# Optimization experiments

Measured on AMD Instinct MI355X. Metric: run time of the kernel, lower is better.

## Reference

```python
import jax, jax.numpy as jnp
import numpy as np

D, T, HID, Q = 33, 49, 64, 64


def _lin(x, w, b):
    return x @ w.T + b


def setup_inputs() -> dict:
    key = jax.random.key(0)
    ks = jax.random.split(key, 40)

    def nrm(k, shape, scale=0.1):
        return jax.random.normal(k, shape, jnp.float32) * scale

    vals = nrm(ks[0], (D, T), 1.0)
    mask = (jax.random.uniform(ks[1], (D, T)) < 0.8).astype(jnp.float32)
    delta = jax.random.uniform(ks[2], (D, T)) * 2.0
    data = jnp.stack([vals, mask, delta])  # [3, 33, 49]

    return {
        "data": data,
        "h0": nrm(ks[3], (HID,), 1.0),
        "H0": nrm(ks[4], (D, HID), 1.0),
        "gh_w": nrm(ks[5], (HID, D)), "gh_b": nrm(ks[6], (HID,)),
        "gst_w": nrm(ks[7], (HID, D)), "gst_b": nrm(ks[8], (HID,)),
        "gru_wih": nrm(ks[9], (3 * HID, D)), "gru_whh": nrm(ks[10], (3 * HID, HID)),
        "gru_bih": nrm(ks[11], (3 * HID,)), "gru_bhh": nrm(ks[12], (3 * HID,)),
        "wu0_w": nrm(ks[13], (Q, HID)), "wu0_b": nrm(ks[14], (Q,)),
        "wu1_w": nrm(ks[15], (Q, 2 * HID)), "wu1_b": nrm(ks[16], (Q,)),
        "wu_w": nrm(ks[17], (Q, 3 * HID)), "wu_b": nrm(ks[18], (Q,)),
        "wh_w": nrm(ks[19], (D, HID + Q)), "wh_b": nrm(ks[20], (D,)),
        "xst_w": nrm(ks[21], (1, HID)), "xst_b": nrm(ks[22], (1,)),
        "wrg_w": nrm(ks[23], (D, HID)),
        "wrs": nrm(ks[24], (1, HID)),
        "tWz": nrm(ks[25], (D, HID, HID)), "tUzx": nrm(ks[26], (D, HID, 1)), "tUzh": nrm(ks[27], (D, HID, HID)),
        "tWr": nrm(ks[28], (D, HID, HID)), "tUrx": nrm(ks[29], (D, HID, 1)), "tUrh": nrm(ks[30], (D, HID, HID)),
        "tWh": nrm(ks[31], (D, HID, HID)), "tUhx": nrm(ks[32], (D, HID, 1)), "tUhh": nrm(ks[33], (D, HID, HID)),
        "tbz": nrm(ks[34], (HID, 1)), "tbr": nrm(ks[35], (HID, 1)), "tbh": nrm(ks[36], (HID, 1)),
    }


def reference(data, h0, H0, gh_w, gh_b, gst_w, gst_b, gru_wih, gru_whh,
              gru_bih, gru_bhh, wu0_w, wu0_b, wu1_w, wu1_b, wu_w, wu_b,
              wh_w, wh_b, xst_w, xst_b, wrg_w, wrs, tWz, tUzx, tUzh,
              tWr, tUrx, tUrh, tWh, tUhx, tUhh, tbz, tbr, tbh):
    X, M, Dt = data[0], data[1], data[2]  # each (33, 49)
    h = h0          # (HID,) -> becomes (1, HID) after first GRUCell step
    H = H0          # (D, HID)
    outs, Hs, xps = [], [], []
    for t in range(T):
        x, m, d = X[:, t], M[:, t], Dt[:, t]
        # GRU-D style decay gate: exp(-max(0, Linear(delta)))
        gamma_h = jnp.exp(-jax.nn.relu(_lin(d, gh_w, gh_b)))
        h = gamma_h * h
        x_st = _lin(H, xst_w, xst_b).reshape(-1)       # (D,)
        x_st_c = m * x + (1 - m) * x_st                # imputed input
        # torch nn.GRUCell
        xi = x_st_c.reshape(1, D)
        hi = h.reshape(1, HID)
        gi = _lin(xi, gru_wih, gru_bih)
        gh_ = _lin(hi, gru_whh, gru_bhh)
        i_r, i_z, i_n = jnp.split(gi, 3, axis=1)
        h_r, h_z, h_n = jnp.split(gh_, 3, axis=1)
        r = jax.nn.sigmoid(i_r + h_r)
        z = jax.nn.sigmoid(i_z + h_z)
        n = jnp.tanh(i_n + r * h_n)
        h = (1 - z) * n + z * hi                       # (1, HID)
        # original detaches the history used for u_t
        outs.append(jax.lax.stop_gradient(h))
        if t == 0:
            u_t = _lin(h0.reshape(1, -1), wu0_w, wu0_b)
        elif t == 1:
            hd = jnp.concatenate([h0.reshape(1, -1), outs[0]], 0).reshape(1, -1)
            u_t = _lin(hd, wu1_w, wu1_b)
        elif t == 2:
            hd = jnp.concatenate([h0.reshape(1, -1), outs[0], outs[1]], 0).reshape(1, -1)
            u_t = _lin(hd, wu_w, wu_b)
        else:
            hd = jnp.concatenate(outs[t - 3:t], 0).reshape(1, -1)
            u_t = _lin(hd, wu_w, wu_b)
        x_gt_hat = _lin(jnp.concatenate([h, u_t], axis=1), wh_w, wh_b)  # (1, D)
        gamma_st = jnp.exp(-jax.nn.relu(_lin(d, gst_w, gst_b)))
        H = gamma_st * H
        # tMGRU cell: per-variable (D=33) batched matmuls
        Hr = H[:, :, None]              # (D, HID, 1)
        xr = x_st_c[:, None, None]      # (D, 1, 1)
        hr = h.reshape(HID, 1)          # (HID, 1)
        z_t = jax.nn.sigmoid(tWz @ Hr + tUzx @ xr + tUzh @ hr + tbz)
        r_t = jax.nn.sigmoid(tWr @ Hr + tUrx @ xr + tUrh @ hr + tbr)
        Hh = jnp.tanh(r_t * (tWh @ Hr) + tUhx @ xr + tUhh @ hr + tbh)
        H = (z_t * Hr + (1 - z_t) * Hh).reshape(D, HID)
        Hs.append(H)
        a = h @ wrg_w.T                 # (1, D)
        b = wrs @ H.T                   # (1, D)
        alpha1 = jax.nn.softmax(a / (a + b), axis=-1)
        alpha2 = jax.nn.softmax(b / (a + b), axis=-1)
        xps.append(alpha1 * x_gt_hat + alpha2 * x_st)  # (1, D)
    H_s = jnp.stack(Hs)                         # (T, D, HID)
    x_pred = jnp.concatenate(xps, axis=0).T     # (D, T)
    return H_s, x_pred
```

## Files before the change

### kernel.cpp

```cpp
#include <hip/hip_runtime.h>
#include <math.h>

#define DD 33
#define TT 49
#define HH 64
#define NB 33
#define NT 256

#define O_WIHT  0
#define O_WHHT  6336
#define O_GH    18624
#define O_GS    21760
#define O_WT0   24896
#define O_WT1   27008
#define O_WTG   31232
#define O_CU    37568
#define O_R     37700
#define O_PF    40936
#define PREP_N  37700

#define SC_AGENT __HIP_MEMORY_SCOPE_AGENT

__device__ __forceinline__ float sigm(float x) {
  return 1.f / (1.f + __expf(-x));
}
__device__ __forceinline__ float ftanh(float x) {
  x = fminf(fmaxf(x, -15.f), 15.f);
  float e = __expf(2.f * x);
  return (e - 1.f) / (e + 1.f);
}

__device__ __forceinline__ float rsum64(float v) {
#pragma unroll
  for (int o = 32; o > 0; o >>= 1) v += __shfl_xor(v, o, 64);
  return v;
}
__device__ __forceinline__ float rmax64(float v) {
#pragma unroll
  for (int o = 32; o > 0; o >>= 1) v = fmaxf(v, __shfl_xor(v, o, 64));
  return v;
}

extern "C" __global__ void gmgru_prep(
    const float* __restrict__ data, const float* __restrict__ gh_w,
    const float* __restrict__ gh_b, const float* __restrict__ gst_w,
    const float* __restrict__ gst_b, const float* __restrict__ wih,
    const float* __restrict__ whh, const float* __restrict__ wu0,
    const float* __restrict__ wu0b, const float* __restrict__ wu1,
    const float* __restrict__ wu1b, const float* __restrict__ wu,
    const float* __restrict__ wub, const float* __restrict__ wh_w,
    float* __restrict__ ws) {
  int idx = blockIdx.x * blockDim.x + threadIdx.x;
  if (idx < 6336) {
    int k = idx / 192, j = idx % 192;
    ws[O_WIHT + idx] = wih[j * DD + k];
  } else if (idx < 18624) {
    int r = idx - 6336, k = r / 192, j = r % 192;
    ws[O_WHHT + r] = whh[j * HH + k];
  } else if (idx < 21760) {
    int r = idx - 18624, t = r / 64, i = r % 64;
    float s = gh_b[i];
    for (int d2 = 0; d2 < DD; ++d2)
      s += data[2 * DD * TT + d2 * TT + t] * gh_w[i * DD + d2];
    ws[O_GH + r] = expf(-fmaxf(s, 0.f));
  } else if (idx < 24896) {
    int r = idx - 21760, t = r / 64, i = r % 64;
    float s = gst_b[i];
    for (int d2 = 0; d2 < DD; ++d2)
      s += data[2 * DD * TT + d2 * TT + t] * gst_w[i * DD + d2];
    ws[O_GS + r] = expf(-fmaxf(s, 0.f));
  } else if (idx < 27008) {
    int r = idx - 24896, dd = r / 64, k = r % 64;
    float s = 0.f;
    for (int q = 0; q < 64; ++q) s += wu0[q * 64 + k] * wh_w[dd * 128 + 64 + q];
    ws[O_WT0 + r] = s;
  } else if (idx < 31232) {
    int r = idx - 27008, dd = r / 128, k = r % 128;
    float s = 0.f;
    for (int q = 0; q < 64; ++q) s += wu1[q * 128 + k] * wh_w[dd * 128 + 64 + q];
    ws[O_WT1 + r] = s;
  } else if (idx < 37568) {
    int r = idx - 31232, dd = r / 192, k = r % 192;
    float s = 0.f;
    for (int q = 0; q < 64; ++q) s += wu[q * 192 + k] * wh_w[dd * 128 + 64 + q];
    ws[O_WTG + r] = s;
  } else if (idx < PREP_N) {
    int r = idx - 37568, dd = r / 4, v = r % 4;
    float s = 0.f;
    if (v < 3) {
      const float* bp = (v == 0) ? wu0b : (v == 1) ? wu1b : wub;
      for (int q = 0; q < 64; ++q) s += bp[q] * wh_w[dd * 128 + 64 + q];
    }
    ws[O_CU + r] = s;
  }
}

extern "C" __global__ void __launch_bounds__(NT, 1)
gmgru_main(const float* __restrict__ data, const float* __restrict__ h0,
           const float* __restrict__ H0, const float* __restrict__ bih,
           const float* __restrict__ bhh, const float* __restrict__ wh_w,
           const float* __restrict__ wh_b, const float* __restrict__ xst_w,
           const float* __restrict__ xst_b, const float* __restrict__ wrg_w,
           const float* __restrict__ wrs, const float* __restrict__ tWz,
           const float* __restrict__ tUzx, const float* __restrict__ tUzh,
           const float* __restrict__ tWr, const float* __restrict__ tUrx,
           const float* __restrict__ tUrh, const float* __restrict__ tWh,
           const float* __restrict__ tUhx, const float* __restrict__ tUhh,
           const float* __restrict__ tbz, const float* __restrict__ tbr,
           const float* __restrict__ tbh, float* __restrict__ ws,
           unsigned long long* __restrict__ pf, float* __restrict__ out) {
  __shared__ __attribute__((aligned(16))) float ubuf[3][4096];
  __shared__ float whhT_l[12288];
  __shared__ float wihT_l[6336];
  __shared__ float partW[3][4][HH], partU[3][4][HH];
  __shared__ float hpreL[HH], hnewL[HH], ghLDS[3 * HH];
  __shared__ float gpre[2][HH];
  __shared__ float xrow[TT], mrow[TT];
  __shared__ float xcddL;

  const int tid = threadIdx.x;
  const int dd = blockIdx.x;
  const int wid = tid >> 6;
  const int lane = tid & 63;

  {
    const float* usrc[3] = {tUzh, tUrh, tUhh};
#pragma unroll 1
    for (int m = 0; m < 3; ++m) {
      const float* s = usrc[m] + dd * 4096;
#pragma unroll
      for (int c = 0; c < 4; ++c) {
        int f = tid * 16 + c * 4;
        float4 v = *reinterpret_cast<const float4*>(s + f);
        int i = f >> 6, k = f & 63;
        *reinterpret_cast<float4*>(&ubuf[m][(k >> 2) * 256 + i * 4]) = v;
      }
    }
  }
  for (int i = tid; i < 12288; i += NT) whhT_l[i] = ws[O_WHHT + i];
  for (int i = tid; i < 6336; i += NT) wihT_l[i] = ws[O_WIHT + i];
  if (tid < HH) {
    gpre[0][tid] = ws[O_GH + tid];
    gpre[1][tid] = ws[O_GS + tid];
  }
  if (tid < TT) {
    xrow[tid] = data[dd * TT + tid];
    mrow[tid] = data[DD * TT + dd * TT + tid];
  }
  const float bih_r = bih[lane];
  const float bih_z = bih[64 + lane];
  const float bih_n = bih[128 + lane];
  const float bhh_r = (tid < 192) ? bhh[tid] : 0.f;
  const float ux0 = tUzx[dd * HH + lane];
  const float ux1 = tUrx[dd * HH + lane];
  const float ux2 = tUhx[dd * HH + lane];
  const float tb0 = tbz[lane];
  const float tb1 = tbr[lane];
  const float tb2 = tbh[lane];
  const float xstw_r = xst_w[lane];
  const float wrg_r = wrg_w[dd * HH + lane];
  const float wrs_r = wrs[lane];
  const float whr0_r = wh_w[dd * 128 + lane];
  const float wtg0_r = ws[O_WTG + dd * 192 + lane];
  const float wtg1_r = ws[O_WTG + dd * 192 + 64 + lane];
  const float wtg2_r = ws[O_WTG + dd * 192 + 128 + lane];
  const float wt0_r = ws[O_WT0 + dd * 64 + lane];
  const float wt1a_r = ws[O_WT1 + dd * 128 + lane];
  const float wt1b_r = ws[O_WT1 + dd * 128 + 64 + lane];
  const float cu0_r = ws[O_CU + dd * 4 + 0];
  const float cu1_r = ws[O_CU + dd * 4 + 1];
  const float cu2_r = ws[O_CU + dd * 4 + 2];
  const float whb_r = wh_b[dd];
  const float xstb_r = xst_b[0];
  const float h0s_r = h0[lane];
  float hprev = h0s_r;
  float Hrow = H0[dd * HH + lane];
  __syncthreads();

  float xst_cur = rsum64(Hrow * xstw_r) + xstb_r;
  if (wid == 0 && lane == 0) {
    float xc0 = mrow[0] * xrow[0] + (1.f - mrow[0]) * xst_cur;
    unsigned long long pk0 =
        (1ULL << 32) | (unsigned long long)__float_as_uint(xc0);
    __hip_atomic_store(&pf[dd], pk0, __ATOMIC_RELAXED, SC_AGENT);
  }
  float xg_m1 = 0.f, xg_m2 = 0.f, xs_m1 = 0.f, xs_m2 = 0.f;
  float h1 = 0.f, h2 = 0.f, h3 = 0.f;

  for (int t = 0; t < TT; ++t) {
    __syncthreads();
    float hpre_r = gpre[0][lane] * hprev;
    float Hdec_r = gpre[1][lane] * Hrow;
    if (wid == 0) hpreL[lane] = hpre_r;
    __syncthreads();

    {
      float pw0 = 0.f, pw1 = 0.f, pw2 = 0.f;
      const int base = dd * 4096 + lane * 64 + wid * 16;
#pragma unroll
      for (int g = 0; g < 4; ++g) {
        float4 a = *reinterpret_cast<const float4*>(tWz + base + g * 4);
        float4 bb = *reinterpret_cast<const float4*>(tWr + base + g * 4);
        float4 c = *reinterpret_cast<const float4*>(tWh + base + g * 4);
        float v0 = __shfl(Hdec_r, wid * 16 + g * 4 + 0, 64);
        float v1 = __shfl(Hdec_r, wid * 16 + g * 4 + 1, 64);
        float v2 = __shfl(Hdec_r, wid * 16 + g * 4 + 2, 64);
        float v3 = __shfl(Hdec_r, wid * 16 + g * 4 + 3, 64);
        pw0 += a.x * v0 + a.y * v1 + a.z * v2 + a.w * v3;
        pw1 += bb.x * v0 + bb.y * v1 + bb.z * v2 + bb.w * v3;
        pw2 += c.x * v0 + c.y * v1 + c.z * v2 + c.w * v3;
      }
      partW[0][wid][lane] = pw0;
      partW[1][wid][lane] = pw1;
      partW[2][wid][lane] = pw2;
    }
    if (tid < 3 * HH) {
      float a0 = 0.f, a1 = 0.f, a2 = 0.f, a3 = 0.f;
#pragma unroll
      for (int k = 0; k < HH; k += 4) {
        a0 += whhT_l[(k + 0) * 192 + tid] * hpreL[k + 0];
        a1 += whhT_l[(k + 1) * 192 + tid] * hpreL[k + 1];
        a2 += whhT_l[(k + 2) * 192 + tid] * hpreL[k + 2];
        a3 += whhT_l[(k + 3) * 192 + tid] * hpreL[k + 3];
      }
      ghLDS[tid] = bhh_r + ((a0 + a1) + (a2 + a3));
    }
    __syncthreads();

    float hn = 0.f;
    if (wid == 0) {
      const unsigned tagv = (unsigned)(t + 1);
      unsigned long long pk;
      for (;;) {
        pk = (lane < NB)
                 ? __hip_atomic_load(&pf[(size_t)t * NB + lane],
                                     __ATOMIC_RELAXED, SC_AGENT)
                 : (((unsigned long long)tagv) << 32);
        if (__all((int)((unsigned)(pk >> 32) == tagv))) break;
        __builtin_amdgcn_s_sleep(1);
      }
      float xcv = __uint_as_float((unsigned)(pk & 0xFFFFFFFFull));
      asm volatile("" ::: "memory");
      float gr = bih_r, gz = bih_z, gn = bih_n;
#pragma unroll
      for (int k = 0; k < DD; ++k) {
        float xk = __shfl(xcv, k, 64);
        gr += wihT_l[k * 192 + lane] * xk;
        gz += wihT_l[k * 192 + 64 + lane] * xk;
        gn += wihT_l[k * 192 + 128 + lane] * xk;
      }
      float rg = sigm(gr + ghLDS[lane]);
      float zg = sigm(gz + ghLDS[64 + lane]);
      float ng = ftanh(gn + rg * ghLDS[128 + lane]);
      hn = (1.f - zg) * ng + zg * hpre_r;
      hnewL[lane] = hn;
      float xcd = __shfl(xcv, dd, 64);
      if (lane == 0) xcddL = xcd;
    }
    __syncthreads();

    {
      float hv[16];
#pragma unroll
      for (int j = 0; j < 16; ++j) hv[j] = hnewL[wid * 16 + j];
      float pu0 = 0.f, pu1 = 0.f, pu2 = 0.f;
#pragma unroll
      for (int g = 0; g < 4; ++g) {
        const int kg = (wid * 4 + g) * 256 + lane * 4;
        float4 a = *reinterpret_cast<const float4*>(&ubuf[0][kg]);
        float4 bb = *reinterpret_cast<const float4*>(&ubuf[1][kg]);
        float4 c = *reinterpret_cast<const float4*>(&ubuf[2][kg]);
        const float v0 = hv[g * 4 + 0], v1 = hv[g * 4 + 1];
        const float v2 = hv[g * 4 + 2], v3 = hv[g * 4 + 3];
        pu0 += a.x * v0 + a.y * v1 + a.z * v2 + a.w * v3;
        pu1 += bb.x * v0 + bb.y * v1 + bb.z * v2 + bb.w * v3;
        pu2 += c.x * v0 + c.y * v1 + c.z * v2 + c.w * v3;
      }
      partU[0][wid][lane] = pu0;
      partU[1][wid][lane] = pu1;
      partU[2][wid][lane] = pu2;
    }
    __syncthreads();

    float r1v = -INFINITY, r2v = -INFINITY;
    if (wid == 1 && t >= 2 && lane < DD) {
      r1v = __hip_atomic_load(&ws[O_R + (t - 2) * 66 + lane], __ATOMIC_RELAXED,
                              SC_AGENT);
      r2v = __hip_atomic_load(&ws[O_R + (t - 2) * 66 + 33 + lane],
                              __ATOMIC_RELAXED, SC_AGENT);
    }

    float sz = partW[0][0][lane] + partW[0][1][lane] + partW[0][2][lane] +
               partW[0][3][lane] + partU[0][0][lane] + partU[0][1][lane] +
               partU[0][2][lane] + partU[0][3][lane];
    float sr = partW[1][0][lane] + partW[1][1][lane] + partW[1][2][lane] +
               partW[1][3][lane] + partU[1][0][lane] + partU[1][1][lane] +
               partU[1][2][lane] + partU[1][3][lane];
    float swh = partW[2][0][lane] + partW[2][1][lane] + partW[2][2][lane] +
                partW[2][3][lane];
    float suh = partU[2][0][lane] + partU[2][1][lane] + partU[2][2][lane] +
                partU[2][3][lane];
    float xc = xcddL;
    float z2 = sigm(sz + ux0 * xc + tb0);
    float r2g = sigm(sr + ux1 * xc + tb1);
    float hh = ftanh(r2g * swh + ux2 * xc + suh + tb2);
    float Hn = z2 * Hdec_r + (1.f - z2) * hh;
    if (wid != 0) hn = hnewL[lane];

    if (wid == 0) {
      float xsn = rsum64(xstw_r * Hn);
      if (lane == 0 && t < TT - 1) {
        float xstv = xsn + xstb_r;
        float xcn = mrow[t + 1] * xrow[t + 1] + (1.f - mrow[t + 1]) * xstv;
        unsigned long long pkn =
            (((unsigned long long)(unsigned)(t + 2)) << 32) |
            (unsigned long long)__float_as_uint(xcn);
        __hip_atomic_store(&pf[(size_t)(t + 1) * NB + dd], pkn,
                           __ATOMIC_RELAXED, SC_AGENT);
      }
    } else if (wid == 1) {
      if (t >= 2) {
        float m1 = rmax64(r1v), m2 = rmax64(r2v);
        float e1 = (lane < DD) ? __expf(r1v - m1) : 0.f;
        float e2 = (lane < DD) ? __expf(r2v - m2) : 0.f;
        float s1 = rsum64(e1), s2 = rsum64(e2);
        float r1o = __shfl(r1v, dd, 64);
        float r2o = __shfl(r2v, dd, 64);
        if (lane == 0) {
          float a1 = __expf(r1o - m1) / s1;
          float a2 = __expf(r2o - m2) / s2;
          out[TT * DD * HH + dd * TT + (t - 2)] = a1 * xg_m2 + a2 * xs_m2;
        }
      }
      float xg = whr0_r * hn;
      if (t == 0) {
        xg += wt0_r * h0s_r;
      } else if (t == 1) {
        xg += wt1a_r * h0s_r + wt1b_r * h1;
      } else if (t == 2) {
        xg += wtg0_r * h0s_r + wtg1_r * h2 + wtg2_r * h1;
      } else {
        xg += wtg0_r * h3 + wtg1_r * h2 + wtg2_r * h1;
      }
      float xgt = rsum64(xg);
      float cu = (t == 0) ? cu0_r : (t == 1) ? cu1_r : cu2_r;
      float xsn1 = rsum64(xstw_r * Hn);
      xg_m2 = xg_m1;
      xs_m2 = xs_m1;
      xg_m1 = xgt + whb_r + cu;
      xs_m1 = xst_cur;
      xst_cur = xsn1 + xstb_r;
      h3 = h2;
      h2 = h1;
      h1 = hn;
    } else if (wid == 2) {
      float av = rsum64(wrg_r * hn);
      float bvv = rsum64(wrs_r * Hn);
      if (lane == 0) {
        float s = av + bvv;
        __hip_atomic_store(&ws[O_R + t * 66 + dd], av / s, __ATOMIC_RELAXED,
                           SC_AGENT);
        __hip_atomic_store(&ws[O_R + t * 66 + 33 + dd], bvv / s,
                           __ATOMIC_RELAXED, SC_AGENT);
      }
      asm volatile("s_waitcnt vmcnt(0)" ::: "memory");
    } else {
      out[t * DD * HH + dd * HH + lane] = Hn;
      if (t + 1 < TT && lane < HH) {
        gpre[0][lane] = ws[O_GH + (t + 1) * HH + lane];
        gpre[1][lane] = ws[O_GS + (t + 1) * HH + lane];
      }
    }
    hprev = hn;
    Hrow = Hn;
  }

  __syncthreads();
  if (wid == 0 && lane == 0) {
    __hip_atomic_store(&pf[(size_t)TT * NB + dd],
                       (((unsigned long long)(unsigned)(TT + 1)) << 32),
                       __ATOMIC_RELAXED, SC_AGENT);
  }
  if (wid == 1) {
    const unsigned tagv = (unsigned)(TT + 1);
    for (;;) {
      unsigned long long pk =
          (lane < NB) ? __hip_atomic_load(&pf[(size_t)TT * NB + lane],
                                          __ATOMIC_RELAXED, SC_AGENT)
                      : (((unsigned long long)tagv) << 32);
      if (__all((int)((unsigned)(pk >> 32) == tagv))) break;
      __builtin_amdgcn_s_sleep(1);
    }
    asm volatile("" ::: "memory");
#pragma unroll 1
    for (int e = 0; e < 2; ++e) {
      const int step = TT - 2 + e;
      float r1v = -INFINITY, r2v = -INFINITY;
      if (lane < DD) {
        r1v = __hip_atomic_load(&ws[O_R + step * 66 + lane], __ATOMIC_RELAXED,
                                SC_AGENT);
        r2v = __hip_atomic_load(&ws[O_R + step * 66 + 33 + lane],
                                __ATOMIC_RELAXED, SC_AGENT);
      }
      float m1 = rmax64(r1v), m2 = rmax64(r2v);
      float e1 = (lane < DD) ? __expf(r1v - m1) : 0.f;
      float e2 = (lane < DD) ? __expf(r2v - m2) : 0.f;
      float s1 = rsum64(e1), s2 = rsum64(e2);
      float r1o = __shfl(r1v, dd, 64);
      float r2o = __shfl(r2v, dd, 64);
      if (lane == 0) {
        float a1 = __expf(r1o - m1) / s1;
        float a2 = __expf(r2o - m2) / s2;
        float xgv = (e == 0) ? xg_m2 : xg_m1;
        float xsv = (e == 0) ? xs_m2 : xs_m1;
        out[TT * DD * HH + dd * TT + step] = a1 * xgv + a2 * xsv;
      }
    }
  }
}

extern "C" void kernel_launch(void* const* d_in, const int* in_sizes, int n_in,
                              void* d_out, int out_size, void* d_ws,
                              size_t ws_size, hipStream_t stream) {
  (void)in_sizes; (void)n_in; (void)out_size; (void)ws_size;
  const float* data   = (const float*)d_in[0];
  const float* h0     = (const float*)d_in[1];
  const float* H0     = (const float*)d_in[2];
  const float* gh_w   = (const float*)d_in[3];
  const float* gh_b   = (const float*)d_in[4];
  const float* gst_w  = (const float*)d_in[5];
  const float* gst_b  = (const float*)d_in[6];
  const float* wih    = (const float*)d_in[7];
  const float* whh    = (const float*)d_in[8];
  const float* bih    = (const float*)d_in[9];
  const float* bhh    = (const float*)d_in[10];
  const float* wu0w   = (const float*)d_in[11];
  const float* wu0b   = (const float*)d_in[12];
  const float* wu1w   = (const float*)d_in[13];
  const float* wu1b   = (const float*)d_in[14];
  const float* wuw    = (const float*)d_in[15];
  const float* wub    = (const float*)d_in[16];
  const float* wh_w   = (const float*)d_in[17];
  const float* wh_b   = (const float*)d_in[18];
  const float* xst_w  = (const float*)d_in[19];
  const float* xst_b  = (const float*)d_in[20];
  const float* wrg_w  = (const float*)d_in[21];
  const float* wrs    = (const float*)d_in[22];
  const float* tWz    = (const float*)d_in[23];
  const float* tUzx   = (const float*)d_in[24];
  const float* tUzh   = (const float*)d_in[25];
  const float* tWr    = (const float*)d_in[26];
  const float* tUrx   = (const float*)d_in[27];
  const float* tUrh   = (const float*)d_in[28];
  const float* tWh    = (const float*)d_in[29];
  const float* tUhx   = (const float*)d_in[30];
  const float* tUhh   = (const float*)d_in[31];
  const float* tbz    = (const float*)d_in[32];
  const float* tbr    = (const float*)d_in[33];
  const float* tbh    = (const float*)d_in[34];

  float* ws = (float*)d_ws;
  unsigned long long* pf = (unsigned long long*)(ws + O_PF);

  hipMemsetAsync(pf, 0, (size_t)(TT + 1) * NB * 8, stream);
  gmgru_prep<<<(PREP_N + 255) / 256, 256, 0, stream>>>(
      data, gh_w, gh_b, gst_w, gst_b, wih, whh, wu0w, wu0b, wu1w, wu1b, wuw,
      wub, wh_w, ws);
  gmgru_main<<<NB, NT, 0, stream>>>(
      data, h0, H0, bih, bhh, wh_w, wh_b, xst_w, xst_b, wrg_w, wrs, tWz, tUzx,
      tUzh, tWr, tUrx, tUrh, tWh, tUhx, tUhh, tbz, tbr, tbh, ws, pf,
      (float*)d_out);
}
```

Before: 202.9 us.

## Aggregate per-step barrier through block 0 and broadcast single flag

Instead of every block polling all 33 per-block slots each step, block 0 alone gathers them with a tight spin (no sleep) and then publishes one per-step flag. The other blocks poll only that flag, then read the slots once. Slots are padded to a stride of 64 per step, and the memset now covers both the slot array and the flag array. This cuts polling traffic on contended cache lines, but adds an extra hop of latency on the serial per-step critical path.

```diff
diff --git a/kernel.cpp b/kernel.cpp
--- a/kernel.cpp
+++ b/kernel.cpp
@@ -17,6 +17,7 @@
 #define O_CU    37568
 #define O_R     37700
 #define O_PF    40936
+#define O_FLG   47336
 #define PREP_N  37700
 
 #define SC_AGENT __HIP_MEMORY_SCOPE_AGENT
@@ -108,7 +109,8 @@
            const float* __restrict__ tUhx, const float* __restrict__ tUhh,
            const float* __restrict__ tbz, const float* __restrict__ tbr,
            const float* __restrict__ tbh, float* __restrict__ ws,
-           unsigned long long* __restrict__ pf, float* __restrict__ out) {
+           unsigned long long* __restrict__ pf, unsigned* __restrict__ flg,
+           float* __restrict__ out) {
   __shared__ __attribute__((aligned(16))) float ubuf[3][4096];
   __shared__ float whhT_l[12288];
   __shared__ float wihT_l[6336];
@@ -230,16 +232,35 @@
     float hn = 0.f;
     if (wid == 0) {
       const unsigned tagv = (unsigned)(t + 1);
-      unsigned long long pk;
-      for (;;) {
-        pk = (lane < NB)
-                 ? __hip_atomic_load(&pf[(size_t)t * NB + lane],
-                                     __ATOMIC_RELAXED, SC_AGENT)
-                 : (((unsigned long long)tagv) << 32);
-        if (__all((int)((unsigned)(pk >> 32) == tagv))) break;
-        __builtin_amdgcn_s_sleep(1);
-      }
-      float xcv = __uint_as_float((unsigned)(pk & 0xFFFFFFFFull));
+      float xcv;
+      if (dd == 0) {
+        unsigned long long pk;
+        for (;;) {
+          pk = (lane < NB)
+                   ? __hip_atomic_load(&pf[(size_t)t * 64 + lane],
+                                       __ATOMIC_RELAXED, SC_AGENT)
+                   : (((unsigned long long)tagv) << 32);
+          if (__all((int)((unsigned)(pk >> 32) == tagv))) break;
+        }
+        if (lane == 0)
+          __hip_atomic_store(&flg[t], tagv, __ATOMIC_RELAXED, SC_AGENT);
+        xcv = __uint_as_float((unsigned)(pk & 0xFFFFFFFFull));
+      } else {
+        for (;;) {
+          unsigned fv = (lane == 0) ? __hip_atomic_load(&flg[t],
+                                                        __ATOMIC_RELAXED,
+                                                        SC_AGENT)
+                                    : 0u;
+          fv = (unsigned)__shfl((int)fv, 0, 64);
+          if (fv == tagv) break;
+          __builtin_amdgcn_s_sleep(1);
+        }
+        unsigned long long pk =
+            (lane < NB) ? __hip_atomic_load(&pf[(size_t)t * 64 + lane],
+                                            __ATOMIC_RELAXED, SC_AGENT)
+                        : 0ULL;
+        xcv = __uint_as_float((unsigned)(pk & 0xFFFFFFFFull));
+      }
       asm volatile("" ::: "memory");
       float gr = bih_r, gz = bih_z, gn = bih_n;
 #pragma unroll
@@ -315,7 +336,7 @@
         unsigned long long pkn =
             (((unsigned long long)(unsigned)(t + 2)) << 32) |
             (unsigned long long)__float_as_uint(xcn);
-        __hip_atomic_store(&pf[(size_t)(t + 1) * NB + dd], pkn,
+        __hip_atomic_store(&pf[(size_t)(t + 1) * 64 + dd], pkn,
                            __ATOMIC_RELAXED, SC_AGENT);
       }
     } else if (wid == 1) {
@@ -377,18 +398,31 @@
 
   __syncthreads();
   if (wid == 0 && lane == 0) {
-    __hip_atomic_store(&pf[(size_t)TT * NB + dd],
+    __hip_atomic_store(&pf[(size_t)TT * 64 + dd],
                        (((unsigned long long)(unsigned)(TT + 1)) << 32),
                        __ATOMIC_RELAXED, SC_AGENT);
+  }
+  if (dd == 0 && wid == 0) {
+    const unsigned tagv = (unsigned)(TT + 1);
+    for (;;) {
+      unsigned long long pk =
+          (lane < NB) ? __hip_atomic_load(&pf[(size_t)TT * 64 + lane],
+                                          __ATOMIC_RELAXED, SC_AGENT)
+                      : (((unsigned long long)tagv) << 32);
+      if (__all((int)((unsigned)(pk >> 32) == tagv))) break;
+    }
+    if (lane == 0)
+      __hip_atomic_store(&flg[TT], tagv, __ATOMIC_RELAXED, SC_AGENT);
   }
   if (wid == 1) {
     const unsigned tagv = (unsigned)(TT + 1);
     for (;;) {
-      unsigned long long pk =
-          (lane < NB) ? __hip_atomic_load(&pf[(size_t)TT * NB + lane],
-                                          __ATOMIC_RELAXED, SC_AGENT)
-                      : (((unsigned long long)tagv) << 32);
-      if (__all((int)((unsigned)(pk >> 32) == tagv))) break;
+      unsigned fv = (lane == 0)
+                        ? __hip_atomic_load(&flg[TT], __ATOMIC_RELAXED,
+                                            SC_AGENT)
+                        : 0u;
+      fv = (unsigned)__shfl((int)fv, 0, 64);
+      if (fv == tagv) break;
       __builtin_amdgcn_s_sleep(1);
     }
     asm volatile("" ::: "memory");
@@ -461,13 +495,15 @@
 
   float* ws = (float*)d_ws;
   unsigned long long* pf = (unsigned long long*)(ws + O_PF);
-
-  hipMemsetAsync(pf, 0, (size_t)(TT + 1) * NB * 8, stream);
+  unsigned* flg = (unsigned*)(ws + O_FLG);
+
+  hipMemsetAsync(pf, 0, (size_t)(TT + 1) * 64 * 8 + (size_t)(TT + 1) * 4,
+                 stream);
   gmgru_prep<<<(PREP_N + 255) / 256, 256, 0, stream>>>(
       data, gh_w, gh_b, gst_w, gst_b, wih, whh, wu0w, wu0b, wu1w, wu1b, wuw,
       wub, wh_w, ws);
   gmgru_main<<<NB, NT, 0, stream>>>(
       data, h0, H0, bih, bhh, wh_w, wh_b, xst_w, xst_b, wrg_w, wrs, tWz, tUzx,
-      tUzh, tWr, tUrx, tUrh, tWh, tUhx, tUhh, tbz, tbr, tbh, ws, pf,
+      tUzh, tWr, tUrx, tUrh, tWh, tUhx, tUhh, tbz, tbr, tbh, ws, pf, flg,
       (float*)d_out);
 }
```

New measurement: 225.6 us. +11.2%, slower.
